# Kernel tuning notes

Measured on AMD Instinct MI355X. Metric: run time of the kernel, lower is better.

Reference implementation:

```python
import jax, jax.numpy as jnp
import numpy as np

D_MODEL = 1024
N_HEADS = 16
HEAD_DIM = D_MODEL // N_HEADS


def setup_inputs() -> dict:
    key = jax.random.key(0)
    kx, kq, kk, kv, ko = jax.random.split(key, 5)
    scale = 1.0 / np.sqrt(D_MODEL)
    x = jax.random.normal(kx, (4, 2048, D_MODEL), dtype=jnp.float32)
    # nn.Linear weights stored as [out, in]; y = x @ W.T
    W_q = jax.random.normal(kq, (D_MODEL, D_MODEL), dtype=jnp.float32) * scale
    W_k = jax.random.normal(kk, (D_MODEL, D_MODEL), dtype=jnp.float32) * scale
    W_v = jax.random.normal(kv, (D_MODEL, D_MODEL), dtype=jnp.float32) * scale
    W_o = jax.random.normal(ko, (D_MODEL, D_MODEL), dtype=jnp.float32) * scale
    return {"x": x, "W_q": W_q, "W_k": W_k, "W_v": W_v, "W_o": W_o}


def reference(x, W_q, W_k, W_v, W_o):
    B, T, C = x.shape
    H, Dh = N_HEADS, HEAD_DIM

    def proj(W):
        return (x @ W.T).reshape(B, T, H, Dh).transpose(0, 2, 1, 3)  # [B,H,T,Dh]

    Q = proj(W_q)
    K = proj(W_q)  # faithful to source bug: K uses W_q, W_k is unused
    V = proj(W_v)

    scores = jnp.einsum('bhqd,bhkd->bhqk', Q, K) / np.sqrt(Dh)
    causal = jnp.tril(jnp.ones((T, T), dtype=bool))
    scores = jnp.where(causal, scores, -jnp.inf)
    attn = jax.nn.softmax(scores, axis=-1)
    out = jnp.einsum('bhqk,bhkd->bhqd', attn, V)
    out = out.transpose(0, 2, 1, 3).reshape(B, T, C)
    return out @ W_o.T
```

## Files before the change

kernel.cpp:

```cpp
#include <hip/hip_runtime.h>
#include <hip/hip_bf16.h>
#include <type_traits>

typedef unsigned short u16;
typedef __attribute__((ext_vector_type(8))) short bf16x8;
typedef __attribute__((ext_vector_type(4))) float f32x4;

#define B_  4
#define T_  2048
#define C_  1024
#define H_  16
#define DH_ 64
#define M_  (B_*T_)

#define GLDS16(g, l) __builtin_amdgcn_global_load_lds( \
    (const __attribute__((address_space(1))) void*)(g), \
    (__attribute__((address_space(3))) void*)(l), 16, 0, 0)

__device__ __forceinline__ u16 f2b(float f) {
  union { __hip_bfloat16 h; u16 u; } cv;
  cv.h = __float2bfloat16(f);
  return cv.u;
}

__global__ void cast_all_kernel(const float* __restrict__ x,  const float* __restrict__ w0,
                                const float* __restrict__ w1, const float* __restrict__ w2,
                                u16* __restrict__ xo, u16* __restrict__ o0,
                                u16* __restrict__ o1, u16* __restrict__ o2) {
  int bid = blockIdx.x;
  const float* src; u16* dst; int blk;
  if (bid < 8192) { src = x; dst = xo; blk = bid; }
  else {
    int k = bid - 8192, w = k >> 10;
    src = (w == 0) ? w0 : (w == 1) ? w1 : w2;
    dst = (w == 0) ? o0 : (w == 1) ? o1 : o2;
    blk = k & 1023;
  }
  int i = (blk * 256 + threadIdx.x) * 4;
  float4 v = *(const float4*)(src + i);
  unsigned lo = (unsigned)f2b(v.x) | ((unsigned)f2b(v.y) << 16);
  unsigned hi = (unsigned)f2b(v.z) | ((unsigned)f2b(v.w) << 16);
  uint2 p; p.x = lo; p.y = hi;
  *(uint2*)(dst + i) = p;
}

__global__ __launch_bounds__(256) void gemm_bt_kernel(
    const u16* __restrict__ A, const u16* __restrict__ Bm,
    void* __restrict__ Cout, int mode)
{
  constexpr int K = 1024;
  __shared__ __align__(16) u16 As[128 * 64];
  __shared__ __align__(16) u16 Bs[128 * 64];

  const int tid  = threadIdx.x;
  const int wave = tid >> 6, lane = tid & 63;
  const int quad = lane >> 4, l15 = lane & 15;
  const int x7   = l15 & 7;
  const int wm = (wave >> 1) * 64, wn = (wave & 1) * 64;
  const int tm = blockIdx.x * 128, tn = blockIdx.y * 128;

  f32x4 acc[4][4] = {};

  for (int k0 = 0; k0 < K; k0 += 64) {
#pragma unroll
    for (int it = 0; it < 4; it++) {
      int ch  = it * 256 + tid;
      int row = ch >> 3;
      int cc  = (ch & 7) ^ (row & 7);
      GLDS16(A  + (size_t)(tm + row) * K + k0 + cc * 8, &As[(it * 256 + wave * 64) * 8]);
      GLDS16(Bm + (size_t)(tn + row) * K + k0 + cc * 8, &Bs[(it * 256 + wave * 64) * 8]);
    }
    __syncthreads();

#pragma unroll
    for (int ks = 0; ks < 2; ks++) {
      bf16x8 af[4], bfr[4];
#pragma unroll
      for (int t = 0; t < 4; t++) {
        int co = ((ks * 4 + quad) ^ x7) * 8;
        af[t]  = *(const bf16x8*)(&As[(wm + t * 16 + l15) * 64 + co]);
        bfr[t] = *(const bf16x8*)(&Bs[(wn + t * 16 + l15) * 64 + co]);
      }
#pragma unroll
      for (int mt = 0; mt < 4; mt++)
#pragma unroll
        for (int nt = 0; nt < 4; nt++)
          acc[mt][nt] = __builtin_amdgcn_mfma_f32_16x16x32_bf16(af[mt], bfr[nt], acc[mt][nt], 0, 0, 0);
    }
    __syncthreads();
  }

  if (mode == 0) {
    u16* out = (u16*)Cout;
    if (tn < 1024) {
#pragma unroll
      for (int mt = 0; mt < 4; mt++)
#pragma unroll
        for (int nt = 0; nt < 4; nt++)
#pragma unroll
          for (int r = 0; r < 4; r++) {
            int gm = tm + wm + mt * 16 + quad * 4 + r;
            int gn = tn + wn + nt * 16 + l15;
            int b = gm >> 11, t = gm & 2047;
            int h = gn >> 6, d = gn & 63;
            out[((size_t)((b * 16 + h) * 2048 + t) << 6) + d] = f2b(acc[mt][nt][r]);
          }
    } else {
#pragma unroll
      for (int mt = 0; mt < 4; mt++)
#pragma unroll
        for (int nt = 0; nt < 4; nt++) {
          int gm0 = tm + wm + mt * 16 + quad * 4;
          int gn  = tn - 1024 + wn + nt * 16 + l15;
          int b = gm0 >> 11, t0 = gm0 & 2047;
          int h = gn >> 6, d = gn & 63;
          alignas(8) u16 tmp[4];
#pragma unroll
          for (int r = 0; r < 4; r++) tmp[r] = f2b(acc[mt][nt][r]);
          *(ushort4*)(out + 8388608 + (((size_t)(b * 16 + h) * 64 + d) << 11) + t0)
              = *(const ushort4*)tmp;
        }
    }
  } else {
    float* out = (float*)Cout;
#pragma unroll
    for (int mt = 0; mt < 4; mt++)
#pragma unroll
      for (int nt = 0; nt < 4; nt++)
#pragma unroll
        for (int r = 0; r < 4; r++) {
          int gm = tm + wm + mt * 16 + quad * 4 + r;
          int gn = tn + wn + nt * 16 + l15;
          out[(size_t)gm * 1024 + gn] = acc[mt][nt][r];
        }
  }
}

__global__ __launch_bounds__(512, 4) void gemm_bt512_kernel(
    const u16* __restrict__ A, const u16* __restrict__ Bm, float* __restrict__ out)
{
  constexpr int K = 1024;
  __shared__ __align__(16) u16 As[128 * 64];
  __shared__ __align__(16) u16 Bs[128 * 64];

  const int tid  = threadIdx.x;
  const int wave = tid >> 6, lane = tid & 63;
  const int quad = lane >> 4, l15 = lane & 15;
  const int x7   = l15 & 7;
  const int wm = (wave >> 1) * 32, wn = (wave & 1) * 64;
  const int tm = blockIdx.x * 128, tn = blockIdx.y * 128;

  f32x4 acc[2][4] = {};

  for (int k0 = 0; k0 < K; k0 += 64) {
#pragma unroll
    for (int it = 0; it < 2; it++) {
      int ch  = it * 512 + tid;
      int row = ch >> 3;
      int cc  = (ch & 7) ^ (row & 7);
      GLDS16(A  + (size_t)(tm + row) * K + k0 + cc * 8, &As[(it * 512 + wave * 64) * 8]);
      GLDS16(Bm + (size_t)(tn + row) * K + k0 + cc * 8, &Bs[(it * 512 + wave * 64) * 8]);
    }
    __syncthreads();

#pragma unroll
    for (int ks = 0; ks < 2; ks++) {
      bf16x8 af[2], bfr[4];
      int co = ((ks * 4 + quad) ^ x7) * 8;
#pragma unroll
      for (int t = 0; t < 2; t++)
        af[t]  = *(const bf16x8*)(&As[(wm + t * 16 + l15) * 64 + co]);
#pragma unroll
      for (int t = 0; t < 4; t++)
        bfr[t] = *(const bf16x8*)(&Bs[(wn + t * 16 + l15) * 64 + co]);
#pragma unroll
      for (int mt = 0; mt < 2; mt++)
#pragma unroll
        for (int nt = 0; nt < 4; nt++)
          acc[mt][nt] = __builtin_amdgcn_mfma_f32_16x16x32_bf16(af[mt], bfr[nt], acc[mt][nt], 0, 0, 0);
    }
    __syncthreads();
  }

#pragma unroll
  for (int mt = 0; mt < 2; mt++)
#pragma unroll
    for (int nt = 0; nt < 4; nt++)
#pragma unroll
      for (int r = 0; r < 4; r++) {
        int gm = tm + wm + mt * 16 + quad * 4 + r;
        int gn = tn + wn + nt * 16 + l15;
        out[(size_t)gm * 1024 + gn] = acc[mt][nt][r];
      }
}

__global__ __launch_bounds__(256, 4) void attn_kernel(
    const u16* __restrict__ Q, const u16* __restrict__ Vt, u16* __restrict__ AO)
{
  constexpr int LDP = 72;
  __shared__ __align__(16) u16 Ks[4096];
  __shared__ __align__(16) u16 Vs[4096];
  __shared__ __align__(16) u16 Ps[4][32 * LDP];

  const int tid  = threadIdx.x;
  const int wave = tid >> 6, lane = tid & 63;
  const int quad = lane >> 4, l15 = lane & 15;
  const int x7   = l15 & 7;
  const int bid  = blockIdx.x;
  const int bh = (bid & 7) * 8 + ((bid >> 3) & 7);
  const int m  = bid >> 6;
  const int i  = (m & 4) ? ((m & 8) ? m - 12 : m + 4) : 15 - m;
  const int b = bh >> 4, h = bh & 15;
  const u16* Qbh = Q  + (size_t)bh * (T_ * DH_);
  const u16* Vbh = Vt + (size_t)bh * (DH_ * T_);
  const int q0w = i * 128 + wave * 32;
  const int kbd = (q0w + 31) >> 6;
  const int nkb = 2 * i + 2;
  u16* myP = &Ps[wave][0];

  const float C1 = 0.18033688f;
  const float C2 = -28.8539008f;
  const bf16x8 ones = { 0x3F80, 0x3F80, 0x3F80, 0x3F80, 0x3F80, 0x3F80, 0x3F80, 0x3F80 };

  bf16x8 qf[2][2];
#pragma unroll
  for (int mt = 0; mt < 2; mt++)
#pragma unroll
    for (int ks = 0; ks < 2; ks++)
      qf[mt][ks] = *(const bf16x8*)(Qbh + (size_t)(q0w + mt * 16 + l15) * DH_ + ks * 32 + quad * 8);

  f32x4 o[2][4] = {};
  f32x4 lsumv[2] = {};

  auto tilecomp = [&](int kb, auto DIAGC) {
    constexpr bool DIAG = decltype(DIAGC)::value;
    const int k0 = kb * 64;
    f32x4 s[2][4] = {};
#pragma unroll
    for (int ks = 0; ks < 2; ks++)
#pragma unroll
      for (int nt = 0; nt < 4; nt++) {
        bf16x8 kf = *(const bf16x8*)(&Ks[(nt * 16 + l15) * 64 + (((ks * 4 + quad) ^ x7) * 8)]);
#pragma unroll
        for (int mt = 0; mt < 2; mt++)
          s[mt][nt] = __builtin_amdgcn_mfma_f32_16x16x32_bf16(qf[mt][ks], kf, s[mt][nt], 0, 0, 0);
      }

#pragma unroll
    for (int mt = 0; mt < 2; mt++)
#pragma unroll
      for (int nt = 0; nt < 4; nt++)
#pragma unroll
        for (int r = 0; r < 4; r++) {
          float p = __builtin_amdgcn_exp2f(s[mt][nt][r] * C1 + C2);
          if constexpr (DIAG) {
            int qg = q0w + mt * 16 + quad * 4 + r;
            int kg = k0 + nt * 16 + l15;
            p = (kg <= qg) ? p : 0.0f;
          }
          myP[(mt * 16 + quad * 4 + r) * LDP + nt * 16 + l15] = f2b(p);
        }

#pragma unroll
    for (int ks2 = 0; ks2 < 2; ks2++) {
      bf16x8 pf[2];
#pragma unroll
      for (int mt = 0; mt < 2; mt++) {
        pf[mt] = *(const bf16x8*)(&myP[(mt * 16 + l15) * LDP + ks2 * 32 + quad * 8]);
        lsumv[mt] = __builtin_amdgcn_mfma_f32_16x16x32_bf16(pf[mt], ones, lsumv[mt], 0, 0, 0);
      }
#pragma unroll
      for (int dt = 0; dt < 4; dt++) {
        bf16x8 vf = *(const bf16x8*)(&Vs[(dt * 16 + l15) * 64 + (((ks2 * 4 + quad) ^ x7) * 8)]);
#pragma unroll
        for (int mt = 0; mt < 2; mt++)
          o[mt][dt] = __builtin_amdgcn_mfma_f32_16x16x32_bf16(pf[mt], vf, o[mt][dt], 0, 0, 0);
      }
    }
  };

  for (int kb = 0; kb < nkb; kb++) {
    const int k0 = kb * 64;
#pragma unroll
    for (int it = 0; it < 2; it++) {
      int ch  = it * 256 + tid;
      int row = ch >> 3;
      int cc  = (ch & 7) ^ (row & 7);
      GLDS16(Qbh + (size_t)(k0 + row) * DH_ + cc * 8, &Ks[(it * 256 + wave * 64) * 8]);
      GLDS16(Vbh + (size_t)row * T_ + k0 + cc * 8,    &Vs[(it * 256 + wave * 64) * 8]);
    }
    __syncthreads();

    if (kb < kbd)        tilecomp(kb, std::false_type{});
    else if (kb == kbd)  tilecomp(kb, std::true_type{});
    __syncthreads();
  }

#pragma unroll
  for (int mt = 0; mt < 2; mt++)
#pragma unroll
    for (int r = 0; r < 4; r++) {
      float rl = 1.0f / lsumv[mt][r];
      int t = q0w + mt * 16 + quad * 4 + r;
#pragma unroll
      for (int dt = 0; dt < 4; dt++)
        AO[((size_t)(b * T_ + t)) * C_ + h * DH_ + dt * 16 + l15] = f2b(o[mt][dt][r] * rl);
    }
}

extern "C" void kernel_launch(void* const* d_in, const int* in_sizes, int n_in,
                              void* d_out, int out_size, void* d_ws, size_t ws_size,
                              hipStream_t stream) {
  (void)in_sizes; (void)n_in; (void)out_size; (void)ws_size;
  const float* x  = (const float*)d_in[0];
  const float* Wq = (const float*)d_in[1];
  const float* Wv = (const float*)d_in[3];
  const float* Wo = (const float*)d_in[4];

  u16* Xb  = (u16*)d_ws;
  u16* AOw = Xb;
  u16* Wqb = Xb  + 8388608;
  u16* Wvb = Wqb + 1048576;
  u16* Wob = Wvb + 1048576;
  u16* Qw  = Wob + 1048576;
  u16* Vtw = Qw  + 8388608;

  cast_all_kernel<<<11264, 256, 0, stream>>>(x, Wq, Wv, Wo, Xb, Wqb, Wvb, Wob);

  gemm_bt_kernel<<<dim3(64, 16), 256, 0, stream>>>(Xb, Wqb, (void*)Qw, 0);

  attn_kernel<<<1024, 256, 0, stream>>>(Qw, Vtw, AOw);

  gemm_bt512_kernel<<<dim3(64, 8), 512, 0, stream>>>(AOw, Wob, (float*)d_out);
}
```

Before: 222.5 us.

## Keep attention probabilities in registers via transposed S and 16x16x16 MFMA

```diff
diff --git a/kernel.cpp b/kernel.cpp
--- a/kernel.cpp
+++ b/kernel.cpp
@@ -4,6 +4,7 @@
 
 typedef unsigned short u16;
 typedef __attribute__((ext_vector_type(8))) short bf16x8;
+typedef __attribute__((ext_vector_type(4))) short bf16x4;
 typedef __attribute__((ext_vector_type(4))) float f32x4;
 
 #define B_  4
@@ -21,6 +22,22 @@
   union { __hip_bfloat16 h; u16 u; } cv;
   cv.h = __float2bfloat16(f);
   return cv.u;
+}
+
+#if defined(__has_builtin)
+#if __has_builtin(__builtin_amdgcn_mfma_f32_16x16x16bf16_1k)
+#define HAVE_MFMA16 1
+#endif
+#endif
+__device__ __forceinline__ f32x4 mfma16(bf16x4 a, bf16x4 b, f32x4 c) {
+#ifdef HAVE_MFMA16
+  return __builtin_amdgcn_mfma_f32_16x16x16bf16_1k(a, b, c, 0, 0, 0);
+#else
+  f32x4 d;
+  asm volatile("v_mfma_f32_16x16x16_bf16 %0, %1, %2, %3\n\ts_nop 7"
+               : "=v"(d) : "v"(a), "v"(b), "v"(c));
+  return d;
+#endif
 }
 
 __global__ void cast_all_kernel(const float* __restrict__ x,  const float* __restrict__ w0,
@@ -194,13 +211,11 @@
       }
 }
 
-__global__ __launch_bounds__(256, 4) void attn_kernel(
+__global__ __launch_bounds__(128, 4) void attn_kernel(
     const u16* __restrict__ Q, const u16* __restrict__ Vt, u16* __restrict__ AO)
 {
-  constexpr int LDP = 72;
   __shared__ __align__(16) u16 Ks[4096];
   __shared__ __align__(16) u16 Vs[4096];
-  __shared__ __align__(16) u16 Ps[4][32 * LDP];
 
   const int tid  = threadIdx.x;
   const int wave = tid >> 6, lane = tid & 63;
@@ -209,18 +224,17 @@
   const int bid  = blockIdx.x;
   const int bh = (bid & 7) * 8 + ((bid >> 3) & 7);
   const int m  = bid >> 6;
-  const int i  = (m & 4) ? ((m & 8) ? m - 12 : m + 4) : 15 - m;
+  const int jj = m >> 2, tt = m & 3;
+  const int i  = (7 - jj) * 4 + ((tt + jj) & 3);
   const int b = bh >> 4, h = bh & 15;
   const u16* Qbh = Q  + (size_t)bh * (T_ * DH_);
   const u16* Vbh = Vt + (size_t)bh * (DH_ * T_);
-  const int q0w = i * 128 + wave * 32;
-  const int kbd = (q0w + 31) >> 6;
-  const int nkb = 2 * i + 2;
-  u16* myP = &Ps[wave][0];
+  const int q0w = i * 64 + wave * 32;
+  const int nkb = i + 1;
 
   const float C1 = 0.18033688f;
   const float C2 = -28.8539008f;
-  const bf16x8 ones = { 0x3F80, 0x3F80, 0x3F80, 0x3F80, 0x3F80, 0x3F80, 0x3F80, 0x3F80 };
+  const bf16x4 ones4 = { 0x3F80, 0x3F80, 0x3F80, 0x3F80 };
 
   bf16x8 qf[2][2];
 #pragma unroll
@@ -235,7 +249,7 @@
   auto tilecomp = [&](int kb, auto DIAGC) {
     constexpr bool DIAG = decltype(DIAGC)::value;
     const int k0 = kb * 64;
-    f32x4 s[2][4] = {};
+    f32x4 st[4][2] = {};
 #pragma unroll
     for (int ks = 0; ks < 2; ks++)
 #pragma unroll
@@ -243,38 +257,37 @@
         bf16x8 kf = *(const bf16x8*)(&Ks[(nt * 16 + l15) * 64 + (((ks * 4 + quad) ^ x7) * 8)]);
 #pragma unroll
         for (int mt = 0; mt < 2; mt++)
-          s[mt][nt] = __builtin_amdgcn_mfma_f32_16x16x32_bf16(qf[mt][ks], kf, s[mt][nt], 0, 0, 0);
+          st[nt][mt] = __builtin_amdgcn_mfma_f32_16x16x32_bf16(kf, qf[mt][ks], st[nt][mt], 0, 0, 0);
       }
 
-#pragma unroll
-    for (int mt = 0; mt < 2; mt++)
-#pragma unroll
-      for (int nt = 0; nt < 4; nt++)
+    bf16x4 pt[4][2];
+#pragma unroll
+    for (int nt = 0; nt < 4; nt++)
+#pragma unroll
+      for (int mt = 0; mt < 2; mt++)
 #pragma unroll
         for (int r = 0; r < 4; r++) {
-          float p = __builtin_amdgcn_exp2f(s[mt][nt][r] * C1 + C2);
+          float p = __builtin_amdgcn_exp2f(st[nt][mt][r] * C1 + C2);
           if constexpr (DIAG) {
-            int qg = q0w + mt * 16 + quad * 4 + r;
-            int kg = k0 + nt * 16 + l15;
+            int kg = k0 + nt * 16 + quad * 4 + r;
+            int qg = q0w + mt * 16 + l15;
             p = (kg <= qg) ? p : 0.0f;
           }
-          myP[(mt * 16 + quad * 4 + r) * LDP + nt * 16 + l15] = f2b(p);
+          pt[nt][mt][r] = (short)f2b(p);
         }
 
 #pragma unroll
-    for (int ks2 = 0; ks2 < 2; ks2++) {
-      bf16x8 pf[2];
-#pragma unroll
-      for (int mt = 0; mt < 2; mt++) {
-        pf[mt] = *(const bf16x8*)(&myP[(mt * 16 + l15) * LDP + ks2 * 32 + quad * 8]);
-        lsumv[mt] = __builtin_amdgcn_mfma_f32_16x16x32_bf16(pf[mt], ones, lsumv[mt], 0, 0, 0);
-      }
+    for (int kc = 0; kc < 4; kc++) {
+#pragma unroll
+      for (int mt = 0; mt < 2; mt++)
+        lsumv[mt] = mfma16(ones4, pt[kc][mt], lsumv[mt]);
 #pragma unroll
       for (int dt = 0; dt < 4; dt++) {
-        bf16x8 vf = *(const bf16x8*)(&Vs[(dt * 16 + l15) * 64 + (((ks2 * 4 + quad) ^ x7) * 8)]);
+        bf16x4 vf = *(const bf16x4*)(&Vs[(dt * 16 + l15) * 64
+                        + (((kc * 2 + (quad >> 1)) ^ x7) * 8) + (quad & 1) * 4]);
 #pragma unroll
         for (int mt = 0; mt < 2; mt++)
-          o[mt][dt] = __builtin_amdgcn_mfma_f32_16x16x32_bf16(pf[mt], vf, o[mt][dt], 0, 0, 0);
+          o[mt][dt] = mfma16(vf, pt[kc][mt], o[mt][dt]);
       }
     }
   };
@@ -282,30 +295,33 @@
   for (int kb = 0; kb < nkb; kb++) {
     const int k0 = kb * 64;
 #pragma unroll
-    for (int it = 0; it < 2; it++) {
-      int ch  = it * 256 + tid;
+    for (int it = 0; it < 4; it++) {
+      int ch  = it * 128 + tid;
       int row = ch >> 3;
       int cc  = (ch & 7) ^ (row & 7);
-      GLDS16(Qbh + (size_t)(k0 + row) * DH_ + cc * 8, &Ks[(it * 256 + wave * 64) * 8]);
-      GLDS16(Vbh + (size_t)row * T_ + k0 + cc * 8,    &Vs[(it * 256 + wave * 64) * 8]);
-    }
-    __syncthreads();
-
-    if (kb < kbd)        tilecomp(kb, std::false_type{});
-    else if (kb == kbd)  tilecomp(kb, std::true_type{});
-    __syncthreads();
-  }
-
-#pragma unroll
-  for (int mt = 0; mt < 2; mt++)
-#pragma unroll
-    for (int r = 0; r < 4; r++) {
-      float rl = 1.0f / lsumv[mt][r];
-      int t = q0w + mt * 16 + quad * 4 + r;
-#pragma unroll
-      for (int dt = 0; dt < 4; dt++)
-        AO[((size_t)(b * T_ + t)) * C_ + h * DH_ + dt * 16 + l15] = f2b(o[mt][dt][r] * rl);
-    }
+      GLDS16(Qbh + (size_t)(k0 + row) * DH_ + cc * 8, &Ks[(it * 128 + wave * 64) * 8]);
+      GLDS16(Vbh + (size_t)row * T_ + k0 + cc * 8,    &Vs[(it * 128 + wave * 64) * 8]);
+    }
+    __syncthreads();
+
+    if (kb < nkb - 1) tilecomp(kb, std::false_type{});
+    else              tilecomp(kb, std::true_type{});
+    __syncthreads();
+  }
+
+#pragma unroll
+  for (int mt = 0; mt < 2; mt++) {
+    float rl = 1.0f / lsumv[mt][0];
+    int t = q0w + mt * 16 + l15;
+#pragma unroll
+    for (int dt = 0; dt < 4; dt++) {
+      alignas(8) u16 tmp[4];
+#pragma unroll
+      for (int r = 0; r < 4; r++) tmp[r] = f2b(o[mt][dt][r] * rl);
+      *(ushort4*)(AO + ((size_t)(b * T_ + t)) * C_ + h * DH_ + dt * 16 + quad * 4)
+          = *(const ushort4*)tmp;
+    }
+  }
 }
 
 extern "C" void kernel_launch(void* const* d_in, const int* in_sizes, int n_in,
@@ -329,7 +345,7 @@
 
   gemm_bt_kernel<<<dim3(64, 16), 256, 0, stream>>>(Xb, Wqb, (void*)Qw, 0);
 
-  attn_kernel<<<1024, 256, 0, stream>>>(Qw, Vtw, AOw);
+  attn_kernel<<<2048, 128, 0, stream>>>(Qw, Vtw, AOw);
 
   gemm_bt512_kernel<<<dim3(64, 8), 512, 0, stream>>>(AOw, Wob, (float*)d_out);
 }
```

After: 431.1 us. +93.7%, slower.

## Halve attention query tile to 64 rows per block, doubling grid

Applied to the files above, without the earlier changes.

```diff
diff --git a/kernel.cpp b/kernel.cpp
--- a/kernel.cpp
+++ b/kernel.cpp
@@ -194,13 +194,13 @@
       }
 }
 
-__global__ __launch_bounds__(256, 4) void attn_kernel(
+__global__ __launch_bounds__(256, 5) void attn_kernel(
     const u16* __restrict__ Q, const u16* __restrict__ Vt, u16* __restrict__ AO)
 {
   constexpr int LDP = 72;
   __shared__ __align__(16) u16 Ks[4096];
   __shared__ __align__(16) u16 Vs[4096];
-  __shared__ __align__(16) u16 Ps[4][32 * LDP];
+  __shared__ __align__(16) u16 Ps[4][16 * LDP];
 
   const int tid  = threadIdx.x;
   const int wave = tid >> 6, lane = tid & 63;
@@ -209,72 +209,60 @@
   const int bid  = blockIdx.x;
   const int bh = (bid & 7) * 8 + ((bid >> 3) & 7);
   const int m  = bid >> 6;
-  const int i  = (m & 4) ? ((m & 8) ? m - 12 : m + 4) : 15 - m;
+  const int jk = m >> 2, m0 = m & 3;
+  const int i  = 31 - 4 * jk - ((jk + m0) & 3);
   const int b = bh >> 4, h = bh & 15;
   const u16* Qbh = Q  + (size_t)bh * (T_ * DH_);
   const u16* Vbh = Vt + (size_t)bh * (DH_ * T_);
-  const int q0w = i * 128 + wave * 32;
-  const int kbd = (q0w + 31) >> 6;
-  const int nkb = 2 * i + 2;
+  const int q0w = i * 64 + wave * 16;
+  const int nkb = i + 1;
   u16* myP = &Ps[wave][0];
 
   const float C1 = 0.18033688f;
   const float C2 = -28.8539008f;
   const bf16x8 ones = { 0x3F80, 0x3F80, 0x3F80, 0x3F80, 0x3F80, 0x3F80, 0x3F80, 0x3F80 };
 
-  bf16x8 qf[2][2];
-#pragma unroll
-  for (int mt = 0; mt < 2; mt++)
-#pragma unroll
-    for (int ks = 0; ks < 2; ks++)
-      qf[mt][ks] = *(const bf16x8*)(Qbh + (size_t)(q0w + mt * 16 + l15) * DH_ + ks * 32 + quad * 8);
-
-  f32x4 o[2][4] = {};
-  f32x4 lsumv[2] = {};
+  bf16x8 qf[2];
+#pragma unroll
+  for (int ks = 0; ks < 2; ks++)
+    qf[ks] = *(const bf16x8*)(Qbh + (size_t)(q0w + l15) * DH_ + ks * 32 + quad * 8);
+
+  f32x4 o[4] = {};
+  f32x4 lsumv = {};
 
   auto tilecomp = [&](int kb, auto DIAGC) {
     constexpr bool DIAG = decltype(DIAGC)::value;
     const int k0 = kb * 64;
-    f32x4 s[2][4] = {};
+    f32x4 s[4] = {};
 #pragma unroll
     for (int ks = 0; ks < 2; ks++)
 #pragma unroll
       for (int nt = 0; nt < 4; nt++) {
         bf16x8 kf = *(const bf16x8*)(&Ks[(nt * 16 + l15) * 64 + (((ks * 4 + quad) ^ x7) * 8)]);
-#pragma unroll
-        for (int mt = 0; mt < 2; mt++)
-          s[mt][nt] = __builtin_amdgcn_mfma_f32_16x16x32_bf16(qf[mt][ks], kf, s[mt][nt], 0, 0, 0);
-      }
-
-#pragma unroll
-    for (int mt = 0; mt < 2; mt++)
-#pragma unroll
-      for (int nt = 0; nt < 4; nt++)
-#pragma unroll
-        for (int r = 0; r < 4; r++) {
-          float p = __builtin_amdgcn_exp2f(s[mt][nt][r] * C1 + C2);
-          if constexpr (DIAG) {
-            int qg = q0w + mt * 16 + quad * 4 + r;
-            int kg = k0 + nt * 16 + l15;
-            p = (kg <= qg) ? p : 0.0f;
-          }
-          myP[(mt * 16 + quad * 4 + r) * LDP + nt * 16 + l15] = f2b(p);
+        s[nt] = __builtin_amdgcn_mfma_f32_16x16x32_bf16(qf[ks], kf, s[nt], 0, 0, 0);
+      }
+
+#pragma unroll
+    for (int nt = 0; nt < 4; nt++)
+#pragma unroll
+      for (int r = 0; r < 4; r++) {
+        float p = __builtin_amdgcn_exp2f(s[nt][r] * C1 + C2);
+        if constexpr (DIAG) {
+          int qg = q0w + quad * 4 + r;
+          int kg = k0 + nt * 16 + l15;
+          p = (kg <= qg) ? p : 0.0f;
         }
+        myP[(quad * 4 + r) * LDP + nt * 16 + l15] = f2b(p);
+      }
 
 #pragma unroll
     for (int ks2 = 0; ks2 < 2; ks2++) {
-      bf16x8 pf[2];
-#pragma unroll
-      for (int mt = 0; mt < 2; mt++) {
-        pf[mt] = *(const bf16x8*)(&myP[(mt * 16 + l15) * LDP + ks2 * 32 + quad * 8]);
-        lsumv[mt] = __builtin_amdgcn_mfma_f32_16x16x32_bf16(pf[mt], ones, lsumv[mt], 0, 0, 0);
-      }
+      bf16x8 pf = *(const bf16x8*)(&myP[l15 * LDP + ks2 * 32 + quad * 8]);
+      lsumv = __builtin_amdgcn_mfma_f32_16x16x32_bf16(pf, ones, lsumv, 0, 0, 0);
 #pragma unroll
       for (int dt = 0; dt < 4; dt++) {
         bf16x8 vf = *(const bf16x8*)(&Vs[(dt * 16 + l15) * 64 + (((ks2 * 4 + quad) ^ x7) * 8)]);
-#pragma unroll
-        for (int mt = 0; mt < 2; mt++)
-          o[mt][dt] = __builtin_amdgcn_mfma_f32_16x16x32_bf16(pf[mt], vf, o[mt][dt], 0, 0, 0);
+        o[dt] = __builtin_amdgcn_mfma_f32_16x16x32_bf16(pf, vf, o[dt], 0, 0, 0);
       }
     }
   };
@@ -291,21 +279,19 @@
     }
     __syncthreads();
 
-    if (kb < kbd)        tilecomp(kb, std::false_type{});
-    else if (kb == kbd)  tilecomp(kb, std::true_type{});
-    __syncthreads();
-  }
-
-#pragma unroll
-  for (int mt = 0; mt < 2; mt++)
-#pragma unroll
-    for (int r = 0; r < 4; r++) {
-      float rl = 1.0f / lsumv[mt][r];
-      int t = q0w + mt * 16 + quad * 4 + r;
-#pragma unroll
-      for (int dt = 0; dt < 4; dt++)
-        AO[((size_t)(b * T_ + t)) * C_ + h * DH_ + dt * 16 + l15] = f2b(o[mt][dt][r] * rl);
-    }
+    if (kb < nkb - 1) tilecomp(kb, std::false_type{});
+    else              tilecomp(kb, std::true_type{});
+    __syncthreads();
+  }
+
+#pragma unroll
+  for (int r = 0; r < 4; r++) {
+    float rl = 1.0f / lsumv[r];
+    int t = q0w + quad * 4 + r;
+#pragma unroll
+    for (int dt = 0; dt < 4; dt++)
+      AO[((size_t)(b * T_ + t)) * C_ + h * DH_ + dt * 16 + l15] = f2b(o[dt][r] * rl);
+  }
 }
 
 extern "C" void kernel_launch(void* const* d_in, const int* in_sizes, int n_in,
@@ -329,7 +315,7 @@
 
   gemm_bt_kernel<<<dim3(64, 16), 256, 0, stream>>>(Xb, Wqb, (void*)Qw, 0);
 
-  attn_kernel<<<1024, 256, 0, stream>>>(Qw, Vtw, AOw);
+  attn_kernel<<<2048, 256, 0, stream>>>(Qw, Vtw, AOw);
 
   gemm_bt512_kernel<<<dim3(64, 8), 512, 0, stream>>>(AOw, Wob, (float*)d_out);
 }
```

Result: slower. 282.7 us (+27.0%).
